# Kernel optimization log

Hardware: AMD Instinct MI355X
Metric: run time of the kernel (lower is better)

## Reference

```python
import jax, jax.numpy as jnp
import numpy as np
from jax.ops import segment_sum

N = 500000
E = 16000000


def _add_self_loops(edge_index, edge_weight, n):
    loop = jnp.arange(n, dtype=edge_index.dtype)
    ei = jnp.concatenate([edge_index, jnp.stack([loop, loop])], axis=1)
    ew = jnp.concatenate([edge_weight, jnp.ones((n,), edge_weight.dtype)])
    return ei, ew


def _gcn_conv(x, edge_index, edge_weight, W, b, n):
    # PyG GCNConv: add self-loops, symmetric normalization, linear, scatter-add, bias
    ei, ew = _add_self_loops(edge_index, edge_weight, n)
    row, col = ei[0], ei[1]
    deg = segment_sum(ew, col, num_segments=n)
    dinv = jnp.where(deg > 0, jax.lax.rsqrt(jnp.maximum(deg, 1e-30)), 0.0)
    norm = dinv[row] * ew * dinv[col]                    # [E+N]
    xw = x @ W                                           # [N, out]
    msg = norm[:, None] * xw[row]                        # gather + scale
    out = segment_sum(msg, col, num_segments=n)          # scatter-add at targets
    return out + b


def setup_inputs() -> dict:
    key = jax.random.key(0)
    k1, k2, k3, k4, k5, k6 = jax.random.split(key, 6)
    x = jax.random.normal(k1, (N, 1), dtype=jnp.float32)
    edge_index = jax.random.randint(k2, (2, E), 0, N, dtype=jnp.int64)
    # Glorot-style init like PyG Linear
    W1 = jax.random.normal(k3, (1, 10), dtype=jnp.float32) * (1.0 / np.sqrt(1))
    b1 = jnp.zeros((10,), dtype=jnp.float32)
    W2 = jax.random.normal(k4, (10, 1), dtype=jnp.float32) * (1.0 / np.sqrt(10))
    b2 = jnp.zeros((1,), dtype=jnp.float32)
    return {"x": x, "edge_index": edge_index, "W1": W1, "b1": b1, "W2": W2, "b2": b2}


def reference(x, edge_index, W1, b1, W2, b2):
    edge_weight = jnp.ones((edge_index.shape[1],), dtype=x.dtype)
    h = _gcn_conv(x, edge_index, edge_weight, W1, b1, N)
    h = jax.nn.relu(h)
    h = _gcn_conv(h, edge_index, edge_weight, W2, b2, N)
    return jnp.clip(h, -0.5, 9.5)
```

## Files before the change

kernel.cpp:

```cpp
#include <hip/hip_runtime.h>


#define SZ      2048
#define BSHIFT  11
#define BMASK   2047u
#define ROWBITS 21
#define ROWMASK ((1u << ROWBITS) - 1u)
#define CHUNK   8192

typedef unsigned u32x4 __attribute__((ext_vector_type(4)));

__global__ __launch_bounds__(256) void gcn_hist(const int* __restrict__ col,
                                                unsigned* __restrict__ H, int e) {
    __shared__ unsigned h[256];
    int c = blockIdx.x, tid = threadIdx.x;
    int lo = c * CHUNK, hi = min(e, lo + CHUNK);
    h[tid] = 0u;
    __syncthreads();
    int nv = (hi - lo) >> 2;
    const int4* cv = (const int4*)(col + lo);
    for (int k = tid; k < nv; k += 256) {
        int4 v = cv[k];
        atomicAdd(&h[((unsigned)v.x) >> BSHIFT], 1u);
        atomicAdd(&h[((unsigned)v.y) >> BSHIFT], 1u);
        atomicAdd(&h[((unsigned)v.z) >> BSHIFT], 1u);
        atomicAdd(&h[((unsigned)v.w) >> BSHIFT], 1u);
    }
    for (int i = lo + (nv << 2) + tid; i < hi; i += 256)
        atomicAdd(&h[((unsigned)col[i]) >> BSHIFT], 1u);
    __syncthreads();
    H[(size_t)c * 256 + tid] = h[tid];
}

__global__ __launch_bounds__(256) void gcn_scan1(unsigned* __restrict__ H,
                                                 unsigned* __restrict__ T, int C) {
    int b = blockIdx.x, tid = threadIdx.x;
    int L = (C + 255) / 256;
    int c0 = tid * L;
    unsigned partial = 0;
    for (int k = 0; k < L; ++k) {
        int c = c0 + k;
        if (c < C) partial += H[(size_t)c * 256 + b];
    }
    __shared__ unsigned s[256];
    s[tid] = partial;
    __syncthreads();
    for (int off = 1; off < 256; off <<= 1) {
        unsigned t = (tid >= off) ? s[tid - off] : 0u;
        __syncthreads();
        s[tid] += t;
        __syncthreads();
    }
    unsigned run = s[tid] - partial;
    for (int k = 0; k < L; ++k) {
        int c = c0 + k;
        if (c < C) {
            unsigned tmp = H[(size_t)c * 256 + b];
            H[(size_t)c * 256 + b] = run;
            run += tmp;
        }
    }
    if (tid == 255) T[b] = s[255];
}

__global__ __launch_bounds__(256) void gcn_scan2(const unsigned* __restrict__ T,
                                                 unsigned* __restrict__ S) {
    int tid = threadIdx.x;
    __shared__ unsigned s[256];
    unsigned v = T[tid];
    s[tid] = v;
    __syncthreads();
    for (int off = 1; off < 256; off <<= 1) {
        unsigned t = (tid >= off) ? s[tid - off] : 0u;
        __syncthreads();
        s[tid] += t;
        __syncthreads();
    }
    S[tid] = s[tid] - v;
}

__global__ __launch_bounds__(512) void gcn_reorder(const int* __restrict__ row,
                                                   const int* __restrict__ col,
                                                   const unsigned* __restrict__ H,
                                                   const unsigned* __restrict__ T,
                                                   const unsigned* __restrict__ S,
                                                   unsigned* __restrict__ sorted,
                                                   int e, int C) {
    __shared__ unsigned keys[CHUNK];
    __shared__ unsigned hist[256], scanL[256], cnt[256], baseG[256];
    int c = blockIdx.x, tid = threadIdx.x;
    int lo = c * CHUNK, hi = min(e, lo + CHUNK), m = hi - lo;
    if (tid < 256) {
        unsigned h0 = H[(size_t)c * 256 + tid];
        unsigned h1 = (c + 1 < C) ? H[(size_t)(c + 1) * 256 + tid] : T[tid];
        unsigned lc = h1 - h0;
        hist[tid]  = lc;
        scanL[tid] = lc;
        cnt[tid]   = 0u;
        baseG[tid] = S[tid] + h0;
    }
    __syncthreads();
    for (int off = 1; off < 256; off <<= 1) {
        unsigned t = 0u;
        if (tid < 256 && tid >= off) t = scanL[tid - off];
        __syncthreads();
        if (tid < 256) scanL[tid] += t;
        __syncthreads();
    }
    if (tid < 256) { scanL[tid] -= hist[tid]; baseG[tid] -= scanL[tid]; }
    __syncthreads();
    int nv = m >> 2;
    const int4* cv = (const int4*)(col + lo);
    const int4* rv = (const int4*)(row + lo);
    for (int k = tid; k < nv; k += 512) {
        int4 cc = cv[k];
        int4 rr = rv[k];
        unsigned b, r;
        b = ((unsigned)cc.x) >> BSHIFT; r = scanL[b] + atomicAdd(&cnt[b], 1u);
        keys[r] = ((((unsigned)cc.x) & BMASK) << ROWBITS) | (unsigned)rr.x;
        b = ((unsigned)cc.y) >> BSHIFT; r = scanL[b] + atomicAdd(&cnt[b], 1u);
        keys[r] = ((((unsigned)cc.y) & BMASK) << ROWBITS) | (unsigned)rr.y;
        b = ((unsigned)cc.z) >> BSHIFT; r = scanL[b] + atomicAdd(&cnt[b], 1u);
        keys[r] = ((((unsigned)cc.z) & BMASK) << ROWBITS) | (unsigned)rr.z;
        b = ((unsigned)cc.w) >> BSHIFT; r = scanL[b] + atomicAdd(&cnt[b], 1u);
        keys[r] = ((((unsigned)cc.w) & BMASK) << ROWBITS) | (unsigned)rr.w;
    }
    for (int i = lo + (nv << 2) + tid; i < hi; i += 512) {
        unsigned cvv = (unsigned)col[i];
        unsigned b = cvv >> BSHIFT;
        unsigned r = scanL[b] + atomicAdd(&cnt[b], 1u);
        keys[r] = ((cvv & BMASK) << ROWBITS) | (unsigned)row[i];
    }
    __syncthreads();
    for (int j = tid; j < m; j += 512) {
        int lo2 = 0, hi2 = 255;
        #pragma unroll
        for (int it = 0; it < 8; ++it) {
            int mid = (lo2 + hi2 + 1) >> 1;
            if (scanL[mid] <= (unsigned)j) lo2 = mid; else hi2 = mid - 1;
        }
        sorted[baseG[lo2] + j] = keys[j];
    }
}

__global__ __launch_bounds__(1024) void gcn_count(const unsigned* __restrict__ sorted,
                                                  const unsigned* __restrict__ S,
                                                  float* __restrict__ P, int npad, int e) {
    __shared__ unsigned acc[SZ];
    int b = blockIdx.x >> 1, g = blockIdx.x & 1, tid = threadIdx.x;
    for (int i = tid; i < SZ; i += 1024) acc[i] = 0u;
    __syncthreads();
    int lo = S[b];
    int hi = (b + 1 < 256) ? (int)S[b + 1] : e;
    int half = (hi - lo + 1) >> 1;
    int mylo = lo + g * half, myhi = min(hi, mylo + half);
    int i0 = min((mylo + 3) & ~3, myhi);
    for (int i = mylo + tid; i < i0; i += 1024)
        atomicAdd(&acc[sorted[i] >> ROWBITS], 1u);
    int nv = (myhi - i0) >> 2;
    const u32x4* sv = (const u32x4*)(sorted + i0);
    for (int k = tid; k < nv; k += 1024) {
        u32x4 v = __builtin_nontemporal_load(&sv[k]);
        atomicAdd(&acc[v[0] >> ROWBITS], 1u);
        atomicAdd(&acc[v[1] >> ROWBITS], 1u);
        atomicAdd(&acc[v[2] >> ROWBITS], 1u);
        atomicAdd(&acc[v[3] >> ROWBITS], 1u);
    }
    for (int i = i0 + (nv << 2) + tid; i < myhi; i += 1024)
        atomicAdd(&acc[sorted[i] >> ROWBITS], 1u);
    __syncthreads();
    size_t off = (size_t)g * npad + (size_t)b * SZ;
    for (int i = tid; i < SZ; i += 1024) P[off + i] = (float)acc[i];
}

__global__ __launch_bounds__(1024) void gcn_gather(const unsigned* __restrict__ sorted,
                                                   const unsigned* __restrict__ S,
                                                   const float* __restrict__ src,
                                                   float* __restrict__ P, int npad, int e) {
    __shared__ float acc[SZ];
    int b = blockIdx.x >> 1, g = blockIdx.x & 1, tid = threadIdx.x;
    for (int i = tid; i < SZ; i += 1024) acc[i] = 0.0f;
    __syncthreads();
    int lo = S[b];
    int hi = (b + 1 < 256) ? (int)S[b + 1] : e;
    int half = (hi - lo + 1) >> 1;
    int mylo = lo + g * half, myhi = min(hi, mylo + half);
    int i0 = min((mylo + 3) & ~3, myhi);
    for (int i = mylo + tid; i < i0; i += 1024) {
        unsigned p = sorted[i];
        atomicAdd(&acc[p >> ROWBITS], src[p & ROWMASK]);
    }
    int nv = (myhi - i0) >> 2;
    const u32x4* sv = (const u32x4*)(sorted + i0);
    for (int k = tid; k < nv; k += 1024) {
        u32x4 v = __builtin_nontemporal_load(&sv[k]);
        float a  = src[v[0] & ROWMASK];
        float bb = src[v[1] & ROWMASK];
        float cc = src[v[2] & ROWMASK];
        float dd = src[v[3] & ROWMASK];
        atomicAdd(&acc[v[0] >> ROWBITS], a);
        atomicAdd(&acc[v[1] >> ROWBITS], bb);
        atomicAdd(&acc[v[2] >> ROWBITS], cc);
        atomicAdd(&acc[v[3] >> ROWBITS], dd);
    }
    for (int i = i0 + (nv << 2) + tid; i < myhi; i += 1024) {
        unsigned p = sorted[i];
        atomicAdd(&acc[p >> ROWBITS], src[p & ROWMASK]);
    }
    __syncthreads();
    size_t off = (size_t)g * npad + (size_t)b * SZ;
    for (int i = tid; i < SZ; i += 1024) P[off + i] = acc[i];
}

__global__ __launch_bounds__(256) void gcn_comb0(const float* __restrict__ P, int npad,
                                                 const float* __restrict__ x,
                                                 float* __restrict__ dinv,
                                                 float* __restrict__ xd, int n) {
    int i = blockIdx.x * 256 + threadIdx.x;
    if (i < n) {
        float d = rsqrtf(1.0f + P[i] + P[(size_t)npad + i]);
        dinv[i] = d;
        xd[i] = d * x[i];
    }
}

__global__ __launch_bounds__(256) void gcn_comb1(const float* __restrict__ P, int npad,
                                                 const float* __restrict__ dinv,
                                                 float* __restrict__ xd,
                                                 const float* __restrict__ W1,
                                                 const float* __restrict__ b1,
                                                 const float* __restrict__ W2, int n) {
    int i = blockIdx.x * 256 + threadIdx.x;
    if (i < n) {
        float d = dinv[i];
        float Sv = d * (P[i] + P[(size_t)npad + i] + xd[i]);
        float t = 0.0f;
        #pragma unroll
        for (int f = 0; f < 10; ++f) {
            float h = fmaf(W1[f], Sv, b1[f]);
            h = h > 0.0f ? h : 0.0f;
            t = fmaf(h, W2[f], t);
        }
        xd[i] = d * t;
    }
}

__global__ __launch_bounds__(256) void gcn_comb2(const float* __restrict__ P, int npad,
                                                 const float* __restrict__ dinv,
                                                 const float* __restrict__ td,
                                                 const float* __restrict__ b2,
                                                 float* __restrict__ out, int n) {
    int i = blockIdx.x * 256 + threadIdx.x;
    if (i < n) {
        float y = b2[0] + dinv[i] * (P[i] + P[(size_t)npad + i] + td[i]);
        out[i] = fminf(fmaxf(y, -0.5f), 9.5f);
    }
}

__global__ void gcn_init(float* deg, float* acc1, float* acc2, int n) {
    int i = blockIdx.x * blockDim.x + threadIdx.x;
    if (i < n) { deg[i] = 1.0f; acc1[i] = 0.0f; acc2[i] = 0.0f; }
}
__global__ void gcn_deg(const int* col, float* deg, int e) {
    int i = blockIdx.x * blockDim.x + threadIdx.x;
    if (i < e) atomicAdd(&deg[col[i]], 1.0f);
}
__global__ void gcn_dinv(const float* x, float* deg_dinv, float* xd, int n) {
    int i = blockIdx.x * blockDim.x + threadIdx.x;
    if (i < n) { float d = rsqrtf(deg_dinv[i]); deg_dinv[i] = d; xd[i] = d * x[i]; }
}
__global__ void gcn_scatter(const int* row, const int* col, const float* v, float* acc, int e) {
    int i = blockIdx.x * blockDim.x + threadIdx.x;
    if (i < e) atomicAdd(&acc[col[i]], v[row[i]]);
}
__global__ void gcn_mid(const float* dinv, const float* xd, float* acc1_td,
                        const float* W1, const float* b1, const float* W2, int n) {
    int i = blockIdx.x * blockDim.x + threadIdx.x;
    if (i < n) {
        float d = dinv[i];
        float Sv = d * (acc1_td[i] + xd[i]);
        float t = 0.0f;
        #pragma unroll
        for (int f = 0; f < 10; ++f) {
            float h = fmaf(W1[f], Sv, b1[f]);
            h = h > 0.0f ? h : 0.0f;
            t = fmaf(h, W2[f], t);
        }
        acc1_td[i] = d * t;
    }
}
__global__ void gcn_final(const float* dinv, const float* td, const float* b2,
                          float* out_acc2, int n) {
    int i = blockIdx.x * blockDim.x + threadIdx.x;
    if (i < n) {
        float y = b2[0] + dinv[i] * (out_acc2[i] + td[i]);
        out_acc2[i] = fminf(fmaxf(y, -0.5f), 9.5f);
    }
}

extern "C" void kernel_launch(void* const* d_in, const int* in_sizes, int n_in,
                              void* d_out, int out_size, void* d_ws, size_t ws_size,
                              hipStream_t stream) {
    const float* x  = (const float*)d_in[0];
    const int*   ei = (const int*)d_in[1];
    const float* W1 = (const float*)d_in[2];
    const float* b1 = (const float*)d_in[3];
    const float* W2 = (const float*)d_in[4];
    const float* b2 = (const float*)d_in[5];

    const int n = in_sizes[0];
    const int e = in_sizes[1] / 2;
    const int* row = ei;
    const int* col = ei + e;
    float* out = (float*)d_out;

    const int nb = (n + SZ - 1) / SZ;
    const int C  = (e + CHUNK - 1) / CHUNK;
    const int npad = nb * SZ;

    size_t need = (size_t)4 * e + (size_t)8 * n + (size_t)8 * npad + 4096;
    bool hFits = (size_t)C * 256 <= (size_t)2 * npad;

    if (ws_size >= need && nb <= 256 && (unsigned)n <= ROWMASK && hFits) {
        unsigned* sorted = (unsigned*)d_ws;
        float*    dinv   = (float*)(sorted + e);
        float*    xd     = dinv + n;
        float*    P      = xd + n;
        unsigned* H      = (unsigned*)P;
        unsigned* T      = (unsigned*)(P + (size_t)2 * npad);
        unsigned* S      = T + 256;

        const int gn = (n + 255) / 256;

        gcn_hist   <<<C,      256, 0, stream>>>(col, H, e);
        gcn_scan1  <<<256,    256, 0, stream>>>(H, T, C);
        gcn_scan2  <<<1,      256, 0, stream>>>(T, S);
        gcn_reorder<<<C,      512, 0, stream>>>(row, col, H, T, S, sorted, e, C);
        gcn_count  <<<nb * 2, 1024, 0, stream>>>(sorted, S, P, npad, e);
        gcn_comb0  <<<gn,     256, 0, stream>>>(P, npad, x, dinv, xd, n);
        gcn_gather <<<nb * 2, 1024, 0, stream>>>(sorted, S, xd, P, npad, e);
        gcn_comb1  <<<gn,     256, 0, stream>>>(P, npad, dinv, xd, W1, b1, W2, n);
        gcn_gather <<<nb * 2, 1024, 0, stream>>>(sorted, S, xd, P, npad, e);
        gcn_comb2  <<<gn,     256, 0, stream>>>(P, npad, dinv, xd, b2, out, n);
    } else {
        float* deg_dinv = (float*)d_ws;
        float* xd       = deg_dinv + n;
        float* acc1     = deg_dinv + 2 * (size_t)n;
        const int B = 256;
        const int gn = (n + B - 1) / B;
        const int ge = (e + B - 1) / B;
        gcn_init   <<<gn, B, 0, stream>>>(deg_dinv, acc1, out, n);
        gcn_deg    <<<ge, B, 0, stream>>>(col, deg_dinv, e);
        gcn_dinv   <<<gn, B, 0, stream>>>(x, deg_dinv, xd, n);
        gcn_scatter<<<ge, B, 0, stream>>>(row, col, xd, acc1, e);
        gcn_mid    <<<gn, B, 0, stream>>>(deg_dinv, xd, acc1, W1, b1, W2, n);
        gcn_scatter<<<ge, B, 0, stream>>>(row, col, acc1, out, e);
        gcn_final  <<<gn, B, 0, stream>>>(deg_dinv, acc1, b2, out, n);
    }
}
```

Before: 447.3 us.

## Add second-level sort by source row block to stage gathers in LDS

Adds a second bucketing pass that sorts each destination-bucket segment by source-row block of 8192 nodes, using a histogram, a scan and a reorder kernel. The gather kernel then stages each 32 KB source block into shared memory and reads from there instead of doing random global loads. This targets the random global gathers in the two propagation passes, at the cost of an extra reorder pass over all edges, an extra edge-sized buffer, and serialized loops over row blocks inside each gather block.

Result: slower. 679.4 us (+51.9%).

```diff
diff --git a/kernel.cpp b/kernel.cpp
--- a/kernel.cpp
+++ b/kernel.cpp
@@ -7,6 +7,9 @@
 #define ROWBITS 21
 #define ROWMASK ((1u << ROWBITS) - 1u)
 #define CHUNK   8192
+#define RBSHIFT 13
+#define RBMASK  8191u
+#define NCH2    32
 
 typedef unsigned u32x4 __attribute__((ext_vector_type(4)));
 
@@ -212,6 +215,141 @@
     for (int i = tid; i < SZ; i += 1024) P[off + i] = acc[i];
 }
 
+__global__ __launch_bounds__(256) void gcn_hist2(const unsigned* __restrict__ sorted1,
+                                                 const unsigned* __restrict__ S,
+                                                 unsigned* __restrict__ H2, int e) {
+    int cb = blockIdx.x >> 5, ch = blockIdx.x & 31, tid = threadIdx.x;
+    int segLo = S[cb];
+    int segHi = (cb + 1 < 256) ? (int)S[cb + 1] : e;
+    int lo = segLo + (ch << 13), hi = min(segHi, lo + 8192);
+    __shared__ unsigned h[64];
+    if (tid < 64) h[tid] = 0u;
+    __syncthreads();
+    for (int i = lo + tid; i < hi; i += 256)
+        atomicAdd(&h[(sorted1[i] & ROWMASK) >> RBSHIFT], 1u);
+    __syncthreads();
+    if (tid < 64) H2[((size_t)cb * NCH2 + ch) * 64 + tid] = h[tid];
+}
+
+__global__ __launch_bounds__(64) void gcn_scan1b(unsigned* __restrict__ H2,
+                                                 const unsigned* __restrict__ S,
+                                                 unsigned* __restrict__ PairOff) {
+    int cb = blockIdx.x, tid = threadIdx.x;
+    unsigned run = 0;
+    for (int ch = 0; ch < NCH2; ++ch) {
+        size_t idx = ((size_t)cb * NCH2 + ch) * 64 + tid;
+        unsigned v = H2[idx];
+        H2[idx] = run;
+        run += v;
+    }
+    __shared__ unsigned s[64];
+    s[tid] = run;
+    __syncthreads();
+    for (int off = 1; off < 64; off <<= 1) {
+        unsigned t = (tid >= off) ? s[tid - off] : 0u;
+        __syncthreads();
+        s[tid] += t;
+        __syncthreads();
+    }
+    PairOff[cb * 64 + tid] = S[cb] + s[tid] - run;
+}
+
+__global__ __launch_bounds__(512) void gcn_reorder2(const unsigned* __restrict__ sorted1,
+                                                    const unsigned* __restrict__ S,
+                                                    const unsigned* __restrict__ H2,
+                                                    const unsigned* __restrict__ PairOff,
+                                                    unsigned* __restrict__ sorted2, int e) {
+    int cb = blockIdx.x >> 5, ch = blockIdx.x & 31, tid = threadIdx.x;
+    int segLo = S[cb];
+    int segHi = (cb + 1 < 256) ? (int)S[cb + 1] : e;
+    int lo = segLo + (ch << 13), hi = min(segHi, lo + 8192);
+    if (lo >= hi) return;
+    __shared__ unsigned keys[8192];
+    __shared__ unsigned short bOf[8192];
+    __shared__ unsigned h[64], scanL[64], cnt[64], baseG[64];
+    int m = hi - lo;
+    unsigned le[16];
+    if (tid < 64) { h[tid] = 0u; cnt[tid] = 0u; }
+    __syncthreads();
+    #pragma unroll
+    for (int q = 0; q < 16; ++q) {
+        int i = lo + tid + q * 512;
+        unsigned k = 0u;
+        if (i < hi) {
+            k = sorted1[i];
+            atomicAdd(&h[(k & ROWMASK) >> RBSHIFT], 1u);
+        }
+        le[q] = k;
+    }
+    __syncthreads();
+    if (tid < 64) scanL[tid] = h[tid];
+    __syncthreads();
+    for (int off = 1; off < 64; off <<= 1) {
+        unsigned t = 0u;
+        if (tid < 64 && tid >= off) t = scanL[tid - off];
+        __syncthreads();
+        if (tid < 64) scanL[tid] += t;
+        __syncthreads();
+    }
+    if (tid < 64) {
+        scanL[tid] -= h[tid];
+        baseG[tid] = PairOff[cb * 64 + tid] + H2[((size_t)cb * NCH2 + ch) * 64 + tid] - scanL[tid];
+    }
+    __syncthreads();
+    #pragma unroll
+    for (int q = 0; q < 16; ++q) {
+        int i = lo + tid + q * 512;
+        if (i < hi) {
+            unsigned k = le[q];
+            unsigned rb = (k & ROWMASK) >> RBSHIFT;
+            unsigned r = scanL[rb] + atomicAdd(&cnt[rb], 1u);
+            keys[r] = k;
+            bOf[r] = (unsigned short)rb;
+        }
+    }
+    __syncthreads();
+    for (int j = tid; j < m; j += 512)
+        sorted2[baseG[bOf[j]] + j] = keys[j];
+}
+
+__global__ __launch_bounds__(1024) void gcn_gather2(const unsigned* __restrict__ sorted2,
+                                                    const unsigned* __restrict__ PairOff,
+                                                    const float* __restrict__ src,
+                                                    float* __restrict__ P, int npad,
+                                                    int n, int nrb) {
+    __shared__ float acc[SZ];
+    __shared__ float stage[8192];
+    int cb = blockIdx.x >> 1, g = blockIdx.x & 1, tid = threadIdx.x;
+    for (int i = tid; i < SZ; i += 1024) acc[i] = 0.0f;
+    int hrb = (nrb + 1) >> 1;
+    int rbLo = g * hrb, rbHi = min(nrb, rbLo + hrb);
+    for (int rb = rbLo; rb < rbHi; ++rb) {
+        int p0 = PairOff[cb * 64 + rb];
+        int p1 = PairOff[cb * 64 + rb + 1];
+        if (p1 <= p0) continue;
+        __syncthreads();
+        int base = rb << RBSHIFT;
+        if (base + 8192 <= n) {
+            const float4* s4 = (const float4*)(src + base);
+            float4* d4 = (float4*)stage;
+            for (int i = tid; i < 2048; i += 1024) d4[i] = s4[i];
+        } else {
+            for (int i = tid; i < 8192; i += 1024) {
+                int idx = base + i;
+                stage[i] = (idx < n) ? src[idx] : 0.0f;
+            }
+        }
+        __syncthreads();
+        for (int i = p0 + tid; i < p1; i += 1024) {
+            unsigned p = sorted2[i];
+            atomicAdd(&acc[p >> ROWBITS], stage[p & RBMASK]);
+        }
+    }
+    __syncthreads();
+    size_t off = (size_t)g * npad + (size_t)cb * SZ;
+    for (int i = tid; i < SZ; i += 1024) P[off + i] = acc[i];
+}
+
 __global__ __launch_bounds__(256) void gcn_comb0(const float* __restrict__ P, int npad,
                                                  const float* __restrict__ x,
                                                  float* __restrict__ dinv,
@@ -317,11 +455,42 @@
     const int nb = (n + SZ - 1) / SZ;
     const int C  = (e + CHUNK - 1) / CHUNK;
     const int npad = nb * SZ;
-
-    size_t need = (size_t)4 * e + (size_t)8 * n + (size_t)8 * npad + 4096;
+    const int nrb = (n + 8191) >> RBSHIFT;
+    const int gn = (n + 255) / 256;
+
     bool hFits = (size_t)C * 256 <= (size_t)2 * npad;
-
-    if (ws_size >= need && nb <= 256 && (unsigned)n <= ROWMASK && hFits) {
+    bool baseOk = nb <= 256 && (unsigned)n <= ROWMASK && hFits;
+
+    size_t need2 = (size_t)8 * e + (size_t)8 * n + (size_t)8 * npad + 2048
+                 + (size_t)nb * NCH2 * 64 * 4 + (size_t)nb * 64 * 4 + 4096;
+    size_t need1 = (size_t)4 * e + (size_t)8 * n + (size_t)8 * npad + 4096;
+
+    if (baseOk && nrb <= 63 && ws_size >= need2) {
+        unsigned* sorted1 = (unsigned*)d_ws;
+        unsigned* sorted2 = sorted1 + e;
+        float*    dinv    = (float*)(sorted2 + e);
+        float*    xd      = dinv + n;
+        float*    P       = xd + n;
+        unsigned* H       = (unsigned*)P;
+        unsigned* T       = (unsigned*)(P + (size_t)2 * npad);
+        unsigned* S       = T + 256;
+        unsigned* H2      = S + 256;
+        unsigned* PairOff = H2 + (size_t)nb * NCH2 * 64;
+
+        gcn_hist    <<<C,        256, 0, stream>>>(col, H, e);
+        gcn_scan1   <<<256,      256, 0, stream>>>(H, T, C);
+        gcn_scan2   <<<1,        256, 0, stream>>>(T, S);
+        gcn_reorder <<<C,        512, 0, stream>>>(row, col, H, T, S, sorted1, e, C);
+        gcn_count   <<<nb * 2,  1024, 0, stream>>>(sorted1, S, P, npad, e);
+        gcn_hist2   <<<nb * NCH2, 256, 0, stream>>>(sorted1, S, H2, e);
+        gcn_scan1b  <<<nb,        64, 0, stream>>>(H2, S, PairOff);
+        gcn_reorder2<<<nb * NCH2, 512, 0, stream>>>(sorted1, S, H2, PairOff, sorted2, e);
+        gcn_comb0   <<<gn,       256, 0, stream>>>(P, npad, x, dinv, xd, n);
+        gcn_gather2 <<<nb * 2,  1024, 0, stream>>>(sorted2, PairOff, xd, P, npad, n, nrb);
+        gcn_comb1   <<<gn,       256, 0, stream>>>(P, npad, dinv, xd, W1, b1, W2, n);
+        gcn_gather2 <<<nb * 2,  1024, 0, stream>>>(sorted2, PairOff, xd, P, npad, n, nrb);
+        gcn_comb2   <<<gn,       256, 0, stream>>>(P, npad, dinv, xd, b2, out, n);
+    } else if (baseOk && ws_size >= need1) {
         unsigned* sorted = (unsigned*)d_ws;
         float*    dinv   = (float*)(sorted + e);
         float*    xd     = dinv + n;
@@ -329,8 +498,6 @@
         unsigned* H      = (unsigned*)P;
         unsigned* T      = (unsigned*)(P + (size_t)2 * npad);
         unsigned* S      = T + 256;
-
-        const int gn = (n + 255) / 256;
 
         gcn_hist   <<<C,      256, 0, stream>>>(col, H, e);
         gcn_scan1  <<<256,    256, 0, stream>>>(H, T, C);
@@ -347,7 +514,6 @@
         float* xd       = deg_dinv + n;
         float* acc1     = deg_dinv + 2 * (size_t)n;
         const int B = 256;
-        const int gn = (n + B - 1) / B;
         const int ge = (e + B - 1) / B;
         gcn_init   <<<gn, B, 0, stream>>>(deg_dinv, acc1, out, n);
         gcn_deg    <<<ge, B, 0, stream>>>(col, deg_dinv, e);
```
